# Kernel tuning notes

Hardware: AMD Instinct MI355X
Metric: run time of the kernel (lower is better)

The kernel has to match this reference:

```python
import jax, jax.numpy as jnp
import numpy as np

B, IMG, P, NP, S = 16, 224, 16, 196, 197
D, H, DH, L, FF = 768, 12, 64, 12, 3072


def setup_inputs() -> dict:
    key = jax.random.key(0)
    ks = jax.random.split(key, 16)
    nrm = lambda k, shape: jax.random.normal(k, shape, jnp.float32) * 0.02
    return {
        "x": jax.random.normal(ks[0], (B, IMG, IMG, 3), jnp.float32),
        "cls": jnp.zeros((1, 1, D), jnp.float32),
        "pos_emb": nrm(ks[1], (S, D)),
        "Wp": nrm(ks[2], (P * P * 3, D)), "bp": jnp.zeros((D,), jnp.float32),
        "Wq": nrm(ks[3], (L, D, D)), "bq": jnp.zeros((L, D), jnp.float32),
        "Wk": nrm(ks[4], (L, D, D)), "bk": jnp.zeros((L, D), jnp.float32),
        "Wv": nrm(ks[5], (L, D, D)), "bv": jnp.zeros((L, D), jnp.float32),
        "Wo": nrm(ks[6], (L, D, D)), "bo": jnp.zeros((L, D), jnp.float32),
        "ln1g": jnp.ones((L, D), jnp.float32), "ln1b": jnp.zeros((L, D), jnp.float32),
        "ln2g": jnp.ones((L, D), jnp.float32), "ln2b": jnp.zeros((L, D), jnp.float32),
        "W1": nrm(ks[7], (L, D, FF)), "b1": jnp.zeros((L, FF), jnp.float32),
        "W2": nrm(ks[8], (L, FF, D)), "b2": jnp.zeros((L, D), jnp.float32),
        "lnfg": jnp.ones((D,), jnp.float32), "lnfb": jnp.zeros((D,), jnp.float32),
    }


def _ln(y, g, b, eps):
    m = y.mean(-1, keepdims=True)
    v = ((y - m) ** 2).mean(-1, keepdims=True)
    return (y - m) / jnp.sqrt(v + eps) * g + b


def _gelu(z):
    # tanh-approx GeLU, exactly as in the source module
    return 0.5 * z * (1.0 + jnp.tanh(np.sqrt(2.0 / np.pi) * (z + 0.044715 * z ** 3)))


def reference(x, cls, pos_emb, Wp, bp, Wq, bq, Wk, bk, Wv, bv, Wo, bo,
              ln1g, ln1b, ln2g, ln2b, W1, b1, W2, b2, lnfg, lnfb):
    Bb = x.shape[0]
    g = IMG // P  # 14 patches per side
    # tf.image.extract_patches with VALID, stride==size: row-major patch flatten
    patches = x.reshape(Bb, g, P, g, P, 3).transpose(0, 1, 3, 2, 4, 5).reshape(Bb, NP, P * P * 3)
    h = patches @ Wp + bp                               # [B, 196, D]
    h = jnp.concatenate([jnp.broadcast_to(cls, (Bb, 1, D)), h], axis=1) + pos_emb  # [B, S, D]

    scale = np.float32(1.0 / np.sqrt(DH))

    def block(h, p):
        wq, bq_, wk, bk_, wv, bv_, wo, bo_, g1, gb1, g2, gb2, w1, b1_, w2, b2_ = p
        y = _ln(h, g1, gb1, 1e-6)
        q = (y @ wq + bq_).reshape(Bb, S, H, DH).transpose(0, 2, 1, 3)  # [B,H,S,dh]
        k = (y @ wk + bk_).reshape(Bb, S, H, DH).transpose(0, 2, 1, 3)
        v = (y @ wv + bv_).reshape(Bb, S, H, DH).transpose(0, 2, 1, 3)
        w = jax.nn.softmax(jnp.einsum('bhqd,bhkd->bhqk', q, k) * scale, axis=-1)
        att = jnp.einsum('bhqk,bhkd->bhqd', w, v)       # [B,H,S,dh]
        # NOTE: in the source the two Permutes cancel, so the "concat" is a raw
        # reshape of the [B,H,S,dh] tensor to [B,S,D] (heads interleaved). Faithful.
        concat = att.reshape(Bb, S, D)
        h1 = h + concat @ wo + bo_
        y = _ln(h1, g2, gb2, 1e-6)
        y = _gelu(y @ w1 + b1_) @ w2 + b2_
        return h1 + y, None

    h, _ = jax.lax.scan(block, h, (Wq, bq, Wk, bk, Wv, bv, Wo, bo,
                                   ln1g, ln1b, ln2g, ln2b, W1, b1, W2, b2))
    return _ln(h, lnfg, lnfb, 1e-3)  # final Keras LayerNorm, default eps=1e-3
```

## Files before the change

kernel.cpp:

```cpp
#include <hip/hip_runtime.h>
#include <cstdint>
#include <cstddef>

#define DD   768
#define HHN  12
#define SS   197
#define FFD  3072
#define MROWS 3152
#define MPAD  3200
#define PROWS 3136
#define PSTRIDE 2457600

typedef __attribute__((ext_vector_type(4))) float  f32x4;
typedef __attribute__((ext_vector_type(8))) __bf16 bf16x8;
typedef __attribute__((ext_vector_type(4))) __bf16 bf16x4;

__global__ __launch_bounds__(256) void w2b_k(const float* __restrict__ W, __bf16* __restrict__ Wb, int N)
{
  __shared__ float Ws[64][65];
  const int t = threadIdx.x;
  const int n0 = blockIdx.x * 64, k0 = blockIdx.y * 64;
  const int nl = t & 63, kq = t >> 6;
  #pragma unroll
  for (int i = 0; i < 16; ++i) {
    const int k = kq * 16 + i;
    Ws[k][nl] = W[(size_t)(k0 + k) * N + n0 + nl];
  }
  __syncthreads();
  #pragma unroll
  for (int r = 0; r < 2; ++r) {
    const int c = r * 256 + t;
    const int kh = c >> 6, n = c & 63;
    bf16x8 v;
    #pragma unroll
    for (int j = 0; j < 8; ++j) v[j] = (__bf16)Ws[kh * 8 + j][n];
    *(bf16x8*)(Wb + ((size_t)((k0 >> 3) + kh) * N + n0 + n) * 8) = v;
  }
}

template<int BN, int NMAT, int MODE, bool GELU_, bool STOREBF, bool VT>
__global__ __launch_bounds__(256) void gemm_k(
    const __bf16* __restrict__ A,
    const __bf16* __restrict__ Bb0, const __bf16* __restrict__ Bb1, const __bf16* __restrict__ Bb2,
    const float* __restrict__ bias0, const float* __restrict__ bias1, const float* __restrict__ bias2,
    float* __restrict__ Cf, __bf16* __restrict__ Cb, __bf16* __restrict__ vt,
    int N, int Kloc, int Kstride)
{
  const int mt = blockIdx.x & 31;
  if (mt >= 25) return;
  const int m0 = mt * 128;
  const int n0 = (blockIdx.x >> 5) * BN;
  const int kz = blockIdx.y;
  const size_t kOff = (size_t)kz * Kloc;

  constexpr int BUFB = (BN == 128) ? 16384 : 12288;
  __shared__ char lds[3 * BUFB];
  const int tid = threadIdx.x;

  int mat = 0, nB = n0, NBw = N;
  const __bf16* Bbp = Bb0; const float* biasp = bias0;
  if (NMAT == 3) {
    mat = n0 / DD; nB = n0 - mat * DD; NBw = DD;
    Bbp   = (mat == 0) ? Bb0   : ((mat == 1) ? Bb1   : Bb2);
    biasp = (mat == 0) ? bias0 : ((mat == 1) ? bias1 : bias2);
  }

  constexpr int NC = (BN == 128) ? 4 : 2;
  f32x4 acc[4][NC];
  const f32x4 z4 = {0.f, 0.f, 0.f, 0.f};
  #pragma unroll
  for (int i = 0; i < 4; ++i)
    #pragma unroll
    for (int j = 0; j < NC; ++j) acc[i][j] = z4;

  const int lane = tid & 63;
  const int wv = tid >> 6;
  const int wr = wv >> 1, wc = wv & 1;
  const int arow = tid & 127, akh = tid >> 7;

  const int nKB = Kloc >> 5;

  auto issue = [&](int kt, int buf) {
    const int k0 = kt << 5;
    char* Ab = lds + buf * BUFB;
    char* Bbl = Ab + 8192;
    {
      const __bf16* ga0 = A + (size_t)(m0 + arow) * Kstride + kOff + k0 + akh * 8;
      auto g0 = (__attribute__((address_space(1))) unsigned int*)(uintptr_t)ga0;
      auto g1 = (__attribute__((address_space(1))) unsigned int*)(uintptr_t)(ga0 + 16);
      auto l0 = (__attribute__((address_space(3))) unsigned int*)(uintptr_t)(Ab + wv * 1024);
      auto l1 = (__attribute__((address_space(3))) unsigned int*)(uintptr_t)(Ab + 4096 + wv * 1024);
      __builtin_amdgcn_global_load_lds(g0, l0, 16, 0, 0);
      __builtin_amdgcn_global_load_lds(g1, l1, 16, 0, 0);
    }
    if (BN == 128) {
      #pragma unroll
      for (int r = 0; r < 2; ++r) {
        const int c = r * 256 + tid;
        const int g = c >> 7, col = c & 127;
        const __bf16* gb = Bbp + ((size_t)(((kOff + k0) >> 3) + g) * NBw + nB + col) * 8;
        auto gp = (__attribute__((address_space(1))) unsigned int*)(uintptr_t)gb;
        auto lp = (__attribute__((address_space(3))) unsigned int*)(uintptr_t)(Bbl + r * 4096 + wv * 1024);
        __builtin_amdgcn_global_load_lds(gp, lp, 16, 0, 0);
      }
    } else {
      const __bf16* gb = Bbp + ((size_t)(((kOff + k0) >> 3) + wv) * NBw + nB + lane) * 8;
      auto gp = (__attribute__((address_space(1))) unsigned int*)(uintptr_t)gb;
      auto lp = (__attribute__((address_space(3))) unsigned int*)(uintptr_t)(Bbl + wv * 1024);
      __builtin_amdgcn_global_load_lds(gp, lp, 16, 0, 0);
    }
  };

  constexpr int WAITIMM = (BN == 128) ? 0xF78  : 0xF76 ;

  issue(0, 0);
  issue(nKB > 1 ? 1 : 0, 1);

  int cb = 0, wb = 2;
  const int q = lane >> 4, r16 = lane & 15;
  for (int kb = 0; kb < nKB; ++kb) {
    __builtin_amdgcn_sched_barrier(0);
    __builtin_amdgcn_s_barrier();
    const int nxt = kb + 2;
    issue(nxt < nKB ? nxt : nKB - 1, wb);
    __builtin_amdgcn_s_waitcnt(WAITIMM);
    __builtin_amdgcn_s_barrier();
    __builtin_amdgcn_sched_barrier(0);

    const char* Ab = lds + cb * BUFB;
    const char* Bbl = Ab + 8192;
    const char* pa = Ab + q * 2048 + (wr * 64 + r16) * 16;
    const char* pb = (BN == 128) ? (Bbl + q * 2048 + (wc * 64 + r16) * 16)
                                 : (Bbl + q * 1024 + (wc * 32 + r16) * 16);
    bf16x8 af[4], bfv[NC];
    #pragma unroll
    for (int i = 0; i < 4; ++i) af[i]  = *(const bf16x8*)(pa + i * 256);
    #pragma unroll
    for (int i = 0; i < NC; ++i) bfv[i] = *(const bf16x8*)(pb + i * 256);
    #pragma unroll
    for (int ri = 0; ri < 4; ++ri)
      #pragma unroll
      for (int ci = 0; ci < NC; ++ci)
        acc[ri][ci] = __builtin_amdgcn_mfma_f32_16x16x32_bf16(af[ri], bfv[ci], acc[ri][ci], 0, 0, 0);

    cb = (cb == 2) ? 0 : cb + 1;
    wb = (wb == 2) ? 0 : wb + 1;
  }
  __builtin_amdgcn_s_waitcnt(0);

  const int q4 = (lane >> 4) * 4, c16 = lane & 15;
  #pragma unroll
  for (int ci = 0; ci < NC; ++ci) {
    const int n = n0 + ((BN == 128) ? wc * 64 : wc * 32) + ci * 16 + c16;
    const float bsv = ((MODE == 1 || MODE == 2) && kz != 0) ? 0.f
                      : biasp[(NMAT == 3) ? (n - mat * DD) : n];
    #pragma unroll
    for (int ri = 0; ri < 4; ++ri) {
      const int mb = m0 + wr * 64 + ri * 16 + q4;
      #pragma unroll
      for (int rg = 0; rg < 4; ++rg) {
        float v = acc[ri][ci][rg] + bsv;
        const int row = mb + rg;
        if (VT && NMAT == 3 && mat == 2) {
          const int b = row / SS;
          if (b < 16) {
            const int s = row - b * SS;
            const int nloc = n - 2 * DD;
            const int hh = nloc >> 6, d = nloc & 63;
            vt[((size_t)(b * HHN + hh) * 28 + (s >> 3)) * 512 + d * 8 + (s & 7)] = (__bf16)v;
          }
        } else {
          const size_t off = (size_t)row * N + n;
          if (MODE == 1) {
            atomicAdd(&Cf[off], v);
          } else if (MODE == 2) {
            Cf[(size_t)kz * PSTRIDE + off] = v;
          } else {
            if (GELU_) {
              const float zz = v;
              const float a = 0.7978845608028654f * (zz + 0.044715f * zz * zz * zz);
              v = 0.5f * zz * (2.0f - 2.0f / (1.0f + __expf(2.0f * a)));
            }
            if (STOREBF) Cb[off] = (__bf16)v; else Cf[off] = v;
          }
        }
      }
    }
  }
}

__global__ __launch_bounds__(256) void attn_k(const __bf16* __restrict__ qkv,
                                              const __bf16* __restrict__ vt,
                                              __bf16* __restrict__ att)
{
  __shared__ char als[58240];
  const int t = threadIdx.x;
  const int qt = blockIdx.x, bh = blockIdx.y;
  const int b = bh / HHN, hh = bh % HHN;
  const int r0 = qt * 64;

  bf16x8 vstage[7];
  #pragma unroll
  for (int i = 0; i < 7; ++i)
    vstage[i] = *(const bf16x8*)(vt + (size_t)bh * 14336 + (size_t)(t + i * 256) * 8);

  #pragma unroll
  for (int i = 0; i < 7; ++i) {
    const int c = t + i * 256;
    const int kh = c & 7, s = c >> 3;
    const int sg = s < SS ? s : (SS - 1);
    const bf16x8 v = *(const bf16x8*)(qkv + (size_t)(b * SS + sg) * 2304 + DD + hh * 64 + kh * 8);
    *(bf16x8*)(als + kh * 3600 + s * 16) = v;
  }
  #pragma unroll
  for (int i = 0; i < 2; ++i) {
    const int c = t + i * 256;
    const int qr = c & 63, dh8 = c >> 6;
    const int rr = r0 + qr;
    const int sg = rr < SS ? rr : (SS - 1);
    const bf16x8 v = *(const bf16x8*)(qkv + (size_t)(b * SS + sg) * 2304 + hh * 64 + dh8 * 8);
    *(bf16x8*)(als + 28800 + dh8 * 1040 + qr * 16) = v;
  }
  __syncthreads();

  const int w = t >> 6, lane = t & 63;
  const int q = lane >> 4, c16 = lane & 15;
  const f32x4 z4 = {0.f, 0.f, 0.f, 0.f};

  f32x4 acc[13];
  #pragma unroll
  for (int nt = 0; nt < 13; ++nt) acc[nt] = z4;
  #pragma unroll
  for (int kk = 0; kk < 2; ++kk) {
    const bf16x8 af = *(const bf16x8*)(als + 28800 + (kk * 4 + q) * 1040 + (w * 16 + c16) * 16);
    #pragma unroll
    for (int nt = 0; nt < 13; ++nt) {
      const bf16x8 bf_ = *(const bf16x8*)(als + (kk * 4 + q) * 3600 + (nt * 16 + c16) * 16);
      acc[nt] = __builtin_amdgcn_mfma_f32_16x16x32_bf16(af, bf_, acc[nt], 0, 0, 0);
    }
  }
  __syncthreads();

  float inv[4];
  #pragma unroll
  for (int rg = 0; rg < 4; ++rg) {
    float mx = -1e30f;
    #pragma unroll
    for (int nt = 0; nt < 13; ++nt) {
      const bool val = (nt < 12) || (c16 < 5);
      const float sv = acc[nt][rg] * 0.125f;
      if (val) mx = fmaxf(mx, sv);
    }
    #pragma unroll
    for (int m = 1; m < 16; m <<= 1) mx = fmaxf(mx, __shfl_xor(mx, m, 16));
    float sm = 0.f;
    #pragma unroll
    for (int nt = 0; nt < 13; ++nt) {
      const bool val = (nt < 12) || (c16 < 5);
      const float e = val ? __expf(acc[nt][rg] * 0.125f - mx) : 0.f;
      acc[nt][rg] = e; sm += e;
    }
    #pragma unroll
    for (int m = 1; m < 16; m <<= 1) sm += __shfl_xor(sm, m, 16);
    inv[rg] = 1.f / sm;
  }

  #pragma unroll
  for (int nt = 0; nt < 14; ++nt) {
    #pragma unroll
    for (int rg = 0; rg < 4; ++rg) {
      const int s = nt * 16 + c16;
      const int qr = w * 16 + q * 4 + rg;
      const float pv = (nt < 13) ? acc[nt][rg] * inv[rg] : 0.f;
      *(__bf16*)(als + (s >> 3) * 1040 + qr * 16 + (s & 7) * 2) = (__bf16)pv;
    }
  }
  #pragma unroll
  for (int i = 0; i < 7; ++i) {
    const int c = t + i * 256;
    *(bf16x8*)(als + 29120 + (c >> 6) * 1040 + (c & 63) * 16) = vstage[i];
  }
  __syncthreads();

  f32x4 o[4];
  #pragma unroll
  for (int dt = 0; dt < 4; ++dt) o[dt] = z4;
  #pragma unroll
  for (int kk = 0; kk < 7; ++kk) {
    const bf16x8 af = *(const bf16x8*)(als + (kk * 4 + q) * 1040 + (w * 16 + c16) * 16);
    #pragma unroll
    for (int dt = 0; dt < 4; ++dt) {
      const bf16x8 bf_ = *(const bf16x8*)(als + 29120 + (kk * 4 + q) * 1040 + (dt * 16 + c16) * 16);
      o[dt] = __builtin_amdgcn_mfma_f32_16x16x32_bf16(af, bf_, o[dt], 0, 0, 0);
    }
  }
  #pragma unroll
  for (int dt = 0; dt < 4; ++dt) {
    #pragma unroll
    for (int rg = 0; rg < 4; ++rg) {
      const int r = r0 + w * 16 + q * 4 + rg;
      if (r < SS)
        att[((size_t)bh * SS + r) * 64 + dt * 16 + c16] = (__bf16)o[dt][rg];
    }
  }
}

template<bool OUTBF>
__global__ __launch_bounds__(256) void ln_k(const float* __restrict__ X,
    const float* __restrict__ g, const float* __restrict__ be, float eps,
    __bf16* __restrict__ Yb, float* __restrict__ Yf)
{
  const int row = blockIdx.x * 4 + (threadIdx.x >> 6), l = threadIdx.x & 63;
  const f32x4* xr = (const f32x4*)(X + (size_t)row * DD);
  f32x4 v[3];
  #pragma unroll
  for (int j = 0; j < 3; ++j) v[j] = xr[l + j * 64];
  float s = 0.f;
  #pragma unroll
  for (int j = 0; j < 3; ++j) s += v[j][0] + v[j][1] + v[j][2] + v[j][3];
  #pragma unroll
  for (int m = 1; m < 64; m <<= 1) s += __shfl_xor(s, m, 64);
  const float mean = s * (1.f / 768.f);
  float vs = 0.f;
  #pragma unroll
  for (int j = 0; j < 3; ++j)
    #pragma unroll
    for (int e = 0; e < 4; ++e) { const float d = v[j][e] - mean; vs += d * d; }
  #pragma unroll
  for (int m = 1; m < 64; m <<= 1) vs += __shfl_xor(vs, m, 64);
  const float rstd = rsqrtf(vs * (1.f / 768.f) + eps);
  const f32x4* gp = (const f32x4*)g; const f32x4* bp = (const f32x4*)be;
  #pragma unroll
  for (int j = 0; j < 3; ++j) {
    const int c4 = l + j * 64;
    const f32x4 gg = gp[c4], bb = bp[c4];
    if (OUTBF) {
      bf16x4 o;
      #pragma unroll
      for (int e = 0; e < 4; ++e) o[e] = (__bf16)((v[j][e] - mean) * rstd * gg[e] + bb[e]);
      *(bf16x4*)(Yb + (size_t)row * DD + c4 * 4) = o;
    } else {
      f32x4 o;
      #pragma unroll
      for (int e = 0; e < 4; ++e) o[e] = (v[j][e] - mean) * rstd * gg[e] + bb[e];
      *(f32x4*)(Yf + (size_t)row * DD + c4 * 4) = o;
    }
  }
}

template<int NPART, bool OUTBF, bool WRITEH>
__global__ __launch_bounds__(256) void lnsum_k(const float* X,
    const float* __restrict__ P, const float* __restrict__ g, const float* __restrict__ be,
    float eps, __bf16* __restrict__ Yb, float* __restrict__ Yf, float* Hout)
{
  const int row = blockIdx.x * 4 + (threadIdx.x >> 6), l = threadIdx.x & 63;
  const f32x4* xr = (const f32x4*)(X + (size_t)row * DD);
  f32x4 v[3];
  #pragma unroll
  for (int j = 0; j < 3; ++j) v[j] = xr[l + j * 64];
  #pragma unroll
  for (int p = 0; p < NPART; ++p) {
    const f32x4* pr = (const f32x4*)(P + (size_t)p * PSTRIDE + (size_t)row * DD);
    #pragma unroll
    for (int j = 0; j < 3; ++j) v[j] += pr[l + j * 64];
  }
  if (WRITEH) {
    f32x4* hw = (f32x4*)(Hout + (size_t)row * DD);
    #pragma unroll
    for (int j = 0; j < 3; ++j) hw[l + j * 64] = v[j];
  }
  float s = 0.f;
  #pragma unroll
  for (int j = 0; j < 3; ++j) s += v[j][0] + v[j][1] + v[j][2] + v[j][3];
  #pragma unroll
  for (int m = 1; m < 64; m <<= 1) s += __shfl_xor(s, m, 64);
  const float mean = s * (1.f / 768.f);
  float vs = 0.f;
  #pragma unroll
  for (int j = 0; j < 3; ++j)
    #pragma unroll
    for (int e = 0; e < 4; ++e) { const float d = v[j][e] - mean; vs += d * d; }
  #pragma unroll
  for (int m = 1; m < 64; m <<= 1) vs += __shfl_xor(vs, m, 64);
  const float rstd = rsqrtf(vs * (1.f / 768.f) + eps);
  const f32x4* gp = (const f32x4*)g; const f32x4* bp = (const f32x4*)be;
  #pragma unroll
  for (int j = 0; j < 3; ++j) {
    const int c4 = l + j * 64;
    const f32x4 gg = gp[c4], bb = bp[c4];
    if (OUTBF) {
      bf16x4 o;
      #pragma unroll
      for (int e = 0; e < 4; ++e) o[e] = (__bf16)((v[j][e] - mean) * rstd * gg[e] + bb[e]);
      *(bf16x4*)(Yb + (size_t)row * DD + c4 * 4) = o;
    } else {
      f32x4 o;
      #pragma unroll
      for (int e = 0; e < 4; ++e) o[e] = (v[j][e] - mean) * rstd * gg[e] + bb[e];
      *(f32x4*)(Yf + (size_t)row * DD + c4 * 4) = o;
    }
  }
}

__global__ __launch_bounds__(256) void im2col_k(const float* __restrict__ x, __bf16* __restrict__ patches)
{
  const int idx = blockIdx.x * 256 + threadIdx.x;
  const int row = idx / 768, col = idx % 768;
  float v = 0.f;
  if (row < PROWS) {
    const int b = row / 196, p = row % 196;
    const int py = p / 14, px = p % 14;
    const int r = col / 48, rem = col % 48, c = rem / 3, ch = rem % 3;
    v = x[((size_t)(b * 224 + py * 16 + r) * 224 + (px * 16 + c)) * 3 + ch];
  }
  patches[idx] = (__bf16)v;
}

__global__ __launch_bounds__(256) void assemble_k(const float* __restrict__ tmp, const float* __restrict__ cls,
    const float* __restrict__ pos, float* __restrict__ h)
{
  const int idx = blockIdx.x * 256 + threadIdx.x;
  const int row = idx / 192, qc = (idx % 192) * 4;
  f32x4 v = {0.f, 0.f, 0.f, 0.f};
  if (row < MROWS) {
    const int b = row / SS, s2 = row % SS;
    if (s2 == 0) v = *(const f32x4*)(cls + qc);
    else         v = *(const f32x4*)(tmp + (size_t)(b * 196 + s2 - 1) * 768 + qc);
    const f32x4 p = *(const f32x4*)(pos + (size_t)s2 * 768 + qc);
    v += p;
  }
  *(f32x4*)(h + (size_t)row * 768 + qc) = v;
}

extern "C" void kernel_launch(void* const* d_in, const int* in_sizes, int n_in,
                              void* d_out, int out_size, void* d_ws, size_t ws_size,
                              hipStream_t stream)
{
  (void)in_sizes; (void)n_in; (void)out_size;
  const float* x    = (const float*)d_in[0];
  const float* cls  = (const float*)d_in[1];
  const float* pos  = (const float*)d_in[2];
  const float* Wp   = (const float*)d_in[3];
  const float* bp   = (const float*)d_in[4];
  const float* Wq   = (const float*)d_in[5];
  const float* bq   = (const float*)d_in[6];
  const float* Wk   = (const float*)d_in[7];
  const float* bk   = (const float*)d_in[8];
  const float* Wv   = (const float*)d_in[9];
  const float* bv   = (const float*)d_in[10];
  const float* Wo   = (const float*)d_in[11];
  const float* bo   = (const float*)d_in[12];
  const float* ln1g = (const float*)d_in[13];
  const float* ln1b = (const float*)d_in[14];
  const float* ln2g = (const float*)d_in[15];
  const float* ln2b = (const float*)d_in[16];
  const float* W1   = (const float*)d_in[17];
  const float* b1   = (const float*)d_in[18];
  const float* W2   = (const float*)d_in[19];
  const float* b2   = (const float*)d_in[20];
  const float* lnfg = (const float*)d_in[21];
  const float* lnfb = (const float*)d_in[22];

  char* ws = (char*)d_ws;
  float*  h    = (float*) (ws + 0);
  __bf16* y    = (__bf16*)(ws + 9830400);
  __bf16* qkv  = (__bf16*)(ws + 14745600);
  float*  tmp  = (float*) (ws + 14745600);
  __bf16* att  = (__bf16*)(ws + 29491200);
  __bf16* mffn = (__bf16*)(ws + 34406400);
  __bf16* patches = (__bf16*)(ws + 34406400);
  __bf16* Wpb = (__bf16*)(ws + 54067200);
  __bf16* Wqb = (__bf16*)(ws + 55246848);
  __bf16* Wkb = (__bf16*)(ws + 69402624);
  __bf16* Wvb = (__bf16*)(ws + 83558400);
  __bf16* Wob = (__bf16*)(ws + 97714176);
  __bf16* W1b = (__bf16*)(ws + 111869952);
  __bf16* W2b = (__bf16*)(ws + 168493056);
  __bf16* vt  = (__bf16*)(ws + 225116160);
  float*  pbuf = (float*)(ws + 230621184);
  if (ws_size < 250281984) return;

  w2b_k<<<dim3(12, 12),  256, 0, stream>>>(Wp, Wpb, DD);
  w2b_k<<<dim3(12, 144), 256, 0, stream>>>(Wq, Wqb, DD);
  w2b_k<<<dim3(12, 144), 256, 0, stream>>>(Wk, Wkb, DD);
  w2b_k<<<dim3(12, 144), 256, 0, stream>>>(Wv, Wvb, DD);
  w2b_k<<<dim3(12, 144), 256, 0, stream>>>(Wo, Wob, DD);
  w2b_k<<<dim3(48, 144), 256, 0, stream>>>(W1, W1b, FFD);
  w2b_k<<<dim3(12, 576), 256, 0, stream>>>(W2, W2b, DD);

  im2col_k<<<MPAD * 768 / 256, 256, 0, stream>>>(x, patches);
  gemm_k<64,1,0,false,false,false><<<12*32, 256, 0, stream>>>(
      patches, Wpb,Wpb,Wpb, bp,bp,bp, tmp, nullptr, nullptr, DD, DD, DD);
  assemble_k<<<MPAD * 192 / 256, 256, 0, stream>>>(tmp, cls, pos, h);

  ln_k<true><<<MROWS / 4, 256, 0, stream>>>(h, ln1g, ln1b, 1e-6f, y, nullptr);
  for (int l = 0; l < 12; ++l) {
    const size_t wDD = (size_t)l * DD * DD, wFF = (size_t)l * DD * FFD;
    gemm_k<128,3,0,false,true,true><<<18*32, 256, 0, stream>>>(
        y, Wqb + wDD, Wkb + wDD, Wvb + wDD,
        bq + l*DD, bk + l*DD, bv + l*DD, nullptr, qkv, vt, 3*DD, DD, DD);
    attn_k<<<dim3(4, 192), 256, 0, stream>>>(qkv, vt, att);
    gemm_k<64,1,2,false,false,false><<<12*32, 256, 0, stream>>>(
        att, Wob + wDD, nullptr, nullptr, bo + l*DD, nullptr, nullptr,
        pbuf, nullptr, nullptr, DD, DD, DD);
    lnsum_k<1,true,true><<<MROWS / 4, 256, 0, stream>>>(
        h, pbuf, ln2g + l*DD, ln2b + l*DD, 1e-6f, y, nullptr, h);
    gemm_k<128,1,0,true,true,false><<<24*32, 256, 0, stream>>>(
        y, W1b + wFF, nullptr, nullptr, b1 + l*FFD, nullptr, nullptr,
        nullptr, mffn, nullptr, FFD, DD, DD);
    gemm_k<128,1,2,false,false,false><<<dim3(6*32, 2), 256, 0, stream>>>(
        mffn, W2b + wFF, nullptr, nullptr, b2 + l*DD, nullptr, nullptr,
        pbuf, nullptr, nullptr, DD, FFD/2, FFD);
    if (l < 11)
      lnsum_k<2,true,true><<<MROWS / 4, 256, 0, stream>>>(
          h, pbuf, ln1g + (l+1)*DD, ln1b + (l+1)*DD, 1e-6f, y, nullptr, h);
  }
  lnsum_k<2,false,false><<<MROWS / 4, 256, 0, stream>>>(
      h, pbuf, lnfg, lnfb, 1e-3f, nullptr, (float*)d_out, nullptr);
}
```

Baseline: 2.439 ms.

## Fuse weight conversion launches and remap GEMM tiles per XCD for L2 locality

```diff
diff --git a/kernel.cpp b/kernel.cpp
--- a/kernel.cpp
+++ b/kernel.cpp
@@ -15,11 +15,28 @@
 typedef __attribute__((ext_vector_type(8))) __bf16 bf16x8;
 typedef __attribute__((ext_vector_type(4))) __bf16 bf16x4;
 
-__global__ __launch_bounds__(256) void w2b_k(const float* __restrict__ W, __bf16* __restrict__ Wb, int N)
+__global__ __launch_bounds__(256) void w2ball_k(
+    const float* __restrict__ Wp, const float* __restrict__ Wq, const float* __restrict__ Wk,
+    const float* __restrict__ Wv, const float* __restrict__ Wo, const float* __restrict__ W1,
+    const float* __restrict__ W2,
+    __bf16* __restrict__ Wpb, __bf16* __restrict__ Wqb, __bf16* __restrict__ Wkb,
+    __bf16* __restrict__ Wvb, __bf16* __restrict__ Wob, __bf16* __restrict__ W1b,
+    __bf16* __restrict__ W2b)
 {
   __shared__ float Ws[64][65];
+  const int bidx = blockIdx.x;
+  const float* W; __bf16* Wb; int NX, loc;
+  if      (bidx <   144) { W = Wp; Wb = Wpb; NX = 12; loc = bidx;         }
+  else if (bidx <  1872) { W = Wq; Wb = Wqb; NX = 12; loc = bidx - 144;   }
+  else if (bidx <  3600) { W = Wk; Wb = Wkb; NX = 12; loc = bidx - 1872;  }
+  else if (bidx <  5328) { W = Wv; Wb = Wvb; NX = 12; loc = bidx - 3600;  }
+  else if (bidx <  7056) { W = Wo; Wb = Wob; NX = 12; loc = bidx - 5328;  }
+  else if (bidx < 13968) { W = W1; Wb = W1b; NX = 48; loc = bidx - 7056;  }
+  else                   { W = W2; Wb = W2b; NX = 12; loc = bidx - 13968; }
+  const int N = NX * 64;
+  const int n0 = (loc % NX) * 64, k0 = (loc / NX) * 64;
+
   const int t = threadIdx.x;
-  const int n0 = blockIdx.x * 64, k0 = blockIdx.y * 64;
   const int nl = t & 63, kq = t >> 6;
   #pragma unroll
   for (int i = 0; i < 16; ++i) {
@@ -46,11 +63,19 @@
     float* __restrict__ Cf, __bf16* __restrict__ Cb, __bf16* __restrict__ vt,
     int N, int Kloc, int Kstride)
 {
-  const int mt = blockIdx.x & 31;
-  if (mt >= 25) return;
-  const int m0 = mt * 128;
-  const int n0 = (blockIdx.x >> 5) * BN;
-  const int kz = blockIdx.y;
+  const int xcd = blockIdx.x & 7;
+  const int ib  = blockIdx.x >> 3;
+  const int NT  = N / BN;
+  const int pm  = xcd >> 1, pn = xcd & 1;
+  const int cm  = 6 + (pm < 1 ? 1 : 0);
+  const int bm  = pm * 6 + (pm < 1 ? pm : 1);
+  const int cn  = NT >> 1;
+  if (ib >= cm * cn) return;
+  const int mt  = bm + ib % cm;
+  const int nt  = pn * cn + ib / cm;
+  const int m0  = mt * 128;
+  const int n0  = nt * BN;
+  const int kz  = blockIdx.y;
   const size_t kOff = (size_t)kz * Kloc;
 
   constexpr int BUFB = (BN == 128) ? 16384 : 12288;
@@ -480,13 +505,8 @@
   float*  pbuf = (float*)(ws + 230621184);
   if (ws_size < 250281984) return;
 
-  w2b_k<<<dim3(12, 12),  256, 0, stream>>>(Wp, Wpb, DD);
-  w2b_k<<<dim3(12, 144), 256, 0, stream>>>(Wq, Wqb, DD);
-  w2b_k<<<dim3(12, 144), 256, 0, stream>>>(Wk, Wkb, DD);
-  w2b_k<<<dim3(12, 144), 256, 0, stream>>>(Wv, Wvb, DD);
-  w2b_k<<<dim3(12, 144), 256, 0, stream>>>(Wo, Wob, DD);
-  w2b_k<<<dim3(48, 144), 256, 0, stream>>>(W1, W1b, FFD);
-  w2b_k<<<dim3(12, 576), 256, 0, stream>>>(W2, W2b, DD);
+  w2ball_k<<<20880, 256, 0, stream>>>(Wp, Wq, Wk, Wv, Wo, W1, W2,
+                                      Wpb, Wqb, Wkb, Wvb, Wob, W1b, W2b);
 
   im2col_k<<<MPAD * 768 / 256, 256, 0, stream>>>(x, patches);
   gemm_k<64,1,0,false,false,false><<<12*32, 256, 0, stream>>>(
```

New measurement: 2.268 ms. 7.0% less time.
